# Optimization experiments

Measured on AMD Instinct MI355X. Metric: run time of the kernel, lower is better.

Reference implementation:

```python
import jax, jax.numpy as jnp
import numpy as np

DIM = 1024
L = 10
C = 1.0
SQRT_C = float(np.sqrt(C))


def _exp_map(x, v, c):
    # Poincare exp map (general form, as in the torch source)
    xn2 = jnp.sum(x * x, axis=-1, keepdims=True)
    lam = 2.0 / (1.0 - c * xn2)
    vn = jnp.sqrt(jnp.sum(v * v, axis=-1, keepdims=True))
    vn = jnp.maximum(vn, 1e-8)
    second = jnp.tanh(SQRT_C * lam * vn / 2.0) / (SQRT_C * vn) * v
    num = (1.0 - c * xn2) * second
    den = (1.0 - 2.0 * c * jnp.sum(x * second, axis=-1, keepdims=True)
           + c * c * xn2 * jnp.sum(second * second, axis=-1, keepdims=True))
    return x + num / den


def _log_map(x, y, c):
    # Poincare log map (general form, as in the torch source)
    xn2 = jnp.sum(x * x, axis=-1, keepdims=True)
    lam = 2.0 / (1.0 - c * xn2)
    yn2 = jnp.sum(y * y, axis=-1, keepdims=True)
    xy = jnp.sum(x * y, axis=-1, keepdims=True)
    tv = (-x * yn2 + y * (1.0 + c * xn2) - 2.0 * c * xy * x) / (1.0 - c * xn2)
    tn = jnp.sqrt(jnp.sum(tv * tv, axis=-1, keepdims=True))
    num = 2.0 * SQRT_C * jnp.arctanh(SQRT_C * tn)
    den = SQRT_C * lam * tn
    return num / den * tv


def _butterfly(u, params):
    # Stage l: blocks of size 2^l along the feature dim; within each block,
    # adjacent pairs are rotated by that block's (a, b) Givens-like rotation.
    # Param layout matches __init__: for layer l there are dim>>l blocks,
    # 2 params (a, b) each, laid out contiguously layer after layer.
    B = u.shape[0]
    offset = 0
    for l in range(L):
        bs = 1 << l
        nb = DIM // bs
        seg = params[offset:offset + 2 * nb]
        offset += 2 * nb
        if bs < 2:
            continue  # block of size 1 has no pair to rotate
        ab = seg.reshape(nb, 2)
        a = ab[:, 0][None, :, None]  # [1, nb, 1]
        b = ab[:, 1][None, :, None]
        u4 = u.reshape(B, nb, bs // 2, 2)
        u0 = u4[..., 0]
        u1 = u4[..., 1]
        u = jnp.stack([a * u0 + b * u1, -b * u0 + a * u1], axis=-1).reshape(B, DIM)
    return u


def setup_inputs() -> dict:
    key = jax.random.key(0)
    k1, k2 = jax.random.split(key)
    # points inside the Poincare ball: per-row norm ~ 0.01*sqrt(1024) ~ 0.32
    x = jax.random.normal(k1, (32768, DIM), dtype=jnp.float32) * 0.01
    P = 2 * sum(DIM >> l for l in range(L))  # 4092
    base = jnp.tile(jnp.array([0.9, 0.0], dtype=jnp.float32), P // 2)
    params = base + 0.1 * jax.random.normal(k2, (P,), dtype=jnp.float32)
    return {"x": x, "params": params}


def reference(x, params):
    u = _log_map(jnp.zeros_like(x), x, C)
    u = _butterfly(u, params)
    return _exp_map(jnp.zeros_like(u), u, C)
```

## Files before the change

### kernel.cpp

```cpp
#include <hip/hip_runtime.h>
#include <math.h>

#define DIM 1024
#define NLEVELS 9
#define ROWS_PER_BLOCK 4
#define NBLOCKS 2048

__global__ __launch_bounds__(256) void hyper_butterfly_fused(
        const float* __restrict__ x,
        const float* __restrict__ params,
        float* __restrict__ out,
        int rows) {
    const int lane = threadIdx.x & 63;
    const int wave = threadIdx.x >> 6;

    float4 W[4];
#pragma unroll
    for (int k = 0; k < 4; ++k) {
        const int base_pair = 2 * (lane + 64 * k);
#pragma unroll
        for (int h = 0; h < 2; ++h) {
            const int p = base_pair + h;
            float wr = 1.0f, wi = 0.0f;
            int off = 2 * DIM;
#pragma unroll
            for (int l = 1; l <= NLEVELS; ++l) {
                const int j = p >> (l - 1);
                const float a = params[off + 2 * j];
                const float b = params[off + 2 * j + 1];
                const float nr = wr * a + wi * b;
                const float ni = wi * a - wr * b;
                wr = nr; wi = ni;
                off += 2 * (DIM >> l);
            }
            if (h == 0) { W[k].x = wr; W[k].y = wi; }
            else        { W[k].z = wr; W[k].w = wi; }
        }
    }

    const int row0 = blockIdx.x * ROWS_PER_BLOCK + wave;
    const int row_stride = gridDim.x * ROWS_PER_BLOCK;

    for (int row = row0; row < rows; row += row_stride) {
        const float4* xrow = (const float4*)(x + (size_t)row * DIM);
        float4 v[4];
#pragma unroll
        for (int k = 0; k < 4; ++k) v[k] = xrow[lane + 64 * k];

        float xn2 = 0.0f;
#pragma unroll
        for (int k = 0; k < 4; ++k)
            xn2 += v[k].x * v[k].x + v[k].y * v[k].y +
                   v[k].z * v[k].z + v[k].w * v[k].w;
#pragma unroll
        for (int m = 32; m > 0; m >>= 1) xn2 += __shfl_xor(xn2, m);

        const float r = sqrtf(xn2);
        const float s1 = (r > 1e-12f)
                             ? (0.5f * logf((1.0f + r) / (1.0f - r)) / r)
                             : 1.0f;

        float un2 = 0.0f;
#pragma unroll
        for (int k = 0; k < 4; ++k) {
            const float ux = s1 * v[k].x, uy = s1 * v[k].y;
            const float uz = s1 * v[k].z, uw = s1 * v[k].w;
            v[k].x = W[k].x * ux - W[k].y * uy;
            v[k].y = W[k].x * uy + W[k].y * ux;
            v[k].z = W[k].z * uz - W[k].w * uw;
            v[k].w = W[k].z * uw + W[k].w * uz;
            un2 += v[k].x * v[k].x + v[k].y * v[k].y +
                   v[k].z * v[k].z + v[k].w * v[k].w;
        }
#pragma unroll
        for (int m = 32; m > 0; m >>= 1) un2 += __shfl_xor(un2, m);

        const float vn = fmaxf(sqrtf(un2), 1e-8f);
        const float s2 = tanhf(vn) / vn;

        float4* orow = (float4*)(out + (size_t)row * DIM);
#pragma unroll
        for (int k = 0; k < 4; ++k) {
            float4 o;
            o.x = s2 * v[k].x; o.y = s2 * v[k].y;
            o.z = s2 * v[k].z; o.w = s2 * v[k].w;
            orow[lane + 64 * k] = o;
        }
    }
}

extern "C" void kernel_launch(void* const* d_in, const int* in_sizes, int n_in,
                              void* d_out, int out_size, void* d_ws, size_t ws_size,
                              hipStream_t stream) {
    const float* x = (const float*)d_in[0];
    const float* params = (const float*)d_in[1];
    float* out = (float*)d_out;

    const int rows = in_sizes[0] / DIM;
    int nblocks = NBLOCKS;
    const int max_needed = (rows + ROWS_PER_BLOCK - 1) / ROWS_PER_BLOCK;
    if (nblocks > max_needed) nblocks = max_needed;

    hyper_butterfly_fused<<<nblocks, 256, 0, stream>>>(x, params, out, rows);
}
```

Baseline: 233.7 us.

## Precompute butterfly weights in separate kernel and merge the two row reductions

The per-pair composite rotation weights are now computed once by a one-block prelude kernel and stored in workspace, so the main kernel no longer recomputes the 9-level chain in every block. The main kernel computes the post-rotation norm algebraically from per-pair weight magnitudes, so both reductions run together and only one cross-lane shuffle pass is needed. The grid-stride loop is replaced by one row per wave with a full grid, and fast __logf/__expf intrinsics replace logf/tanhf. The cost is a second kernel launch, dependence on workspace, and slightly reduced precision from the fast math intrinsics.

```diff
diff --git a/kernel.cpp b/kernel.cpp
--- a/kernel.cpp
+++ b/kernel.cpp
@@ -2,90 +2,94 @@
 #include <math.h>
 
 #define DIM 1024
+#define NPAIRS 512
 #define NLEVELS 9
-#define ROWS_PER_BLOCK 4
-#define NBLOCKS 2048
+#define PAR_OFF (2 * DIM)
 
-__global__ __launch_bounds__(256) void hyper_butterfly_fused(
+__global__ void butterfly_weights_kernel(const float* __restrict__ params,
+                                         float2* __restrict__ w) {
+#pragma unroll
+    for (int h = 0; h < 2; ++h) {
+        const int p = threadIdx.x + 256 * h;
+        float wr = 1.0f, wi = 0.0f;
+        int off = PAR_OFF;
+#pragma unroll
+        for (int l = 1; l <= NLEVELS; ++l) {
+            const int j = p >> (l - 1);
+            const float a = params[off + 2 * j];
+            const float b = params[off + 2 * j + 1];
+            const float nr = wr * a + wi * b;
+            const float ni = wi * a - wr * b;
+            wr = nr; wi = ni;
+            off += 2 * (DIM >> l);
+        }
+        w[p] = make_float2(wr, wi);
+    }
+}
+
+__global__ __launch_bounds__(256) void hyper_butterfly_main(
         const float* __restrict__ x,
-        const float* __restrict__ params,
+        const float4* __restrict__ w4,
         float* __restrict__ out,
         int rows) {
     const int lane = threadIdx.x & 63;
     const int wave = threadIdx.x >> 6;
+    const int row = blockIdx.x * 4 + wave;
+    if (row >= rows) return;
 
-    float4 W[4];
+    const float4* xrow = (const float4*)(x + (size_t)row * DIM);
+    float4 v[4], W[4];
+#pragma unroll
+    for (int k = 0; k < 4; ++k) v[k] = xrow[lane + 64 * k];
+#pragma unroll
+    for (int k = 0; k < 4; ++k) W[k] = w4[lane + 64 * k];
+
+    float xn2 = 0.0f, t = 0.0f;
 #pragma unroll
     for (int k = 0; k < 4; ++k) {
-        const int base_pair = 2 * (lane + 64 * k);
+        const float n0 = v[k].x * v[k].x + v[k].y * v[k].y;
+        const float n1 = v[k].z * v[k].z + v[k].w * v[k].w;
+        const float a0 = W[k].x * W[k].x + W[k].y * W[k].y;
+        const float a1 = W[k].z * W[k].z + W[k].w * W[k].w;
+        xn2 += n0 + n1;
+        t   += a0 * n0 + a1 * n1;
+    }
 #pragma unroll
-        for (int h = 0; h < 2; ++h) {
-            const int p = base_pair + h;
-            float wr = 1.0f, wi = 0.0f;
-            int off = 2 * DIM;
-#pragma unroll
-            for (int l = 1; l <= NLEVELS; ++l) {
-                const int j = p >> (l - 1);
-                const float a = params[off + 2 * j];
-                const float b = params[off + 2 * j + 1];
-                const float nr = wr * a + wi * b;
-                const float ni = wi * a - wr * b;
-                wr = nr; wi = ni;
-                off += 2 * (DIM >> l);
-            }
-            if (h == 0) { W[k].x = wr; W[k].y = wi; }
-            else        { W[k].z = wr; W[k].w = wi; }
-        }
+    for (int m = 32; m > 0; m >>= 1) {
+        xn2 += __shfl_xor(xn2, m);
+        t   += __shfl_xor(t, m);
     }
 
-    const int row0 = blockIdx.x * ROWS_PER_BLOCK + wave;
-    const int row_stride = gridDim.x * ROWS_PER_BLOCK;
+    float4 y[4];
+#pragma unroll
+    for (int k = 0; k < 4; ++k) {
+        y[k].x = W[k].x * v[k].x - W[k].y * v[k].y;
+        y[k].y = W[k].x * v[k].y + W[k].y * v[k].x;
+        y[k].z = W[k].z * v[k].z - W[k].w * v[k].w;
+        y[k].w = W[k].z * v[k].w + W[k].w * v[k].z;
+    }
 
-    for (int row = row0; row < rows; row += row_stride) {
-        const float4* xrow = (const float4*)(x + (size_t)row * DIM);
-        float4 v[4];
+    const float r = sqrtf(xn2);
+    const float s1 = (r > 1e-12f)
+                         ? (0.5f * __logf((1.0f + r) / (1.0f - r)) / r)
+                         : 1.0f;
+    float vn = fmaxf(s1 * sqrtf(t), 1e-8f);
+    float s2;
+    if (vn < 1e-4f) {
+        s2 = 1.0f - vn * vn * (1.0f / 3.0f);
+    } else {
+        const float e = __expf(2.0f * vn);
+        s2 = (e - 1.0f) / ((e + 1.0f) * vn);
+    }
+    const float sc = s1 * s2;
+
+    float4* orow = (float4*)(out + (size_t)row * DIM);
 #pragma unroll
-        for (int k = 0; k < 4; ++k) v[k] = xrow[lane + 64 * k];
-
-        float xn2 = 0.0f;
-#pragma unroll
-        for (int k = 0; k < 4; ++k)
-            xn2 += v[k].x * v[k].x + v[k].y * v[k].y +
-                   v[k].z * v[k].z + v[k].w * v[k].w;
-#pragma unroll
-        for (int m = 32; m > 0; m >>= 1) xn2 += __shfl_xor(xn2, m);
-
-        const float r = sqrtf(xn2);
-        const float s1 = (r > 1e-12f)
-                             ? (0.5f * logf((1.0f + r) / (1.0f - r)) / r)
-                             : 1.0f;
-
-        float un2 = 0.0f;
-#pragma unroll
-        for (int k = 0; k < 4; ++k) {
-            const float ux = s1 * v[k].x, uy = s1 * v[k].y;
-            const float uz = s1 * v[k].z, uw = s1 * v[k].w;
-            v[k].x = W[k].x * ux - W[k].y * uy;
-            v[k].y = W[k].x * uy + W[k].y * ux;
-            v[k].z = W[k].z * uz - W[k].w * uw;
-            v[k].w = W[k].z * uw + W[k].w * uz;
-            un2 += v[k].x * v[k].x + v[k].y * v[k].y +
-                   v[k].z * v[k].z + v[k].w * v[k].w;
-        }
-#pragma unroll
-        for (int m = 32; m > 0; m >>= 1) un2 += __shfl_xor(un2, m);
-
-        const float vn = fmaxf(sqrtf(un2), 1e-8f);
-        const float s2 = tanhf(vn) / vn;
-
-        float4* orow = (float4*)(out + (size_t)row * DIM);
-#pragma unroll
-        for (int k = 0; k < 4; ++k) {
-            float4 o;
-            o.x = s2 * v[k].x; o.y = s2 * v[k].y;
-            o.z = s2 * v[k].z; o.w = s2 * v[k].w;
-            orow[lane + 64 * k] = o;
-        }
+    for (int k = 0; k < 4; ++k) {
+        float4 o;
+        o.x = sc * y[k].x; o.y = sc * y[k].y;
+        o.z = sc * y[k].z; o.w = sc * y[k].w;
+        orow[lane + 64 * k] = o;
     }
 }
 
@@ -95,11 +99,11 @@
     const float* x = (const float*)d_in[0];
     const float* params = (const float*)d_in[1];
     float* out = (float*)d_out;
+    float2* w = (float2*)d_ws;
 
     const int rows = in_sizes[0] / DIM;
-    int nblocks = NBLOCKS;
-    const int max_needed = (rows + ROWS_PER_BLOCK - 1) / ROWS_PER_BLOCK;
-    if (nblocks > max_needed) nblocks = max_needed;
+    const int nblocks = (rows + 3) / 4;
 
-    hyper_butterfly_fused<<<nblocks, 256, 0, stream>>>(x, params, out, rows);
+    butterfly_weights_kernel<<<1, 256, 0, stream>>>(params, w);
+    hyper_butterfly_main<<<nblocks, 256, 0, stream>>>(x, (const float4*)w, out, rows);
 }
```

Result: no change. 231.2 us (-1.0%).
